# Kernel optimization log

Hardware: AMD Instinct MI355X
Metric: run time of the kernel (lower is better)

## Reference

```python
import jax, jax.numpy as jnp
import numpy as np

ATT_SCALE = 1.0

def setup_inputs() -> dict:
    key = jax.random.key(0)
    ks = jax.random.split(key, 9)
    N, Cin, Cout, E = 50000, 512, 512, 400000
    x = jax.random.normal(ks[0], (N, Cin), dtype=jnp.float32)
    eb = jax.random.randint(ks[1], (2, E), 0, N, dtype=jnp.int32)
    ev = jax.random.randint(ks[2], (2, E), 0, N, dtype=jnp.int32)
    ec = jax.random.randint(ks[3], (2, E), 0, N, dtype=jnp.int32)
    s = 1.0 / np.sqrt(Cin)
    W_bond = jax.random.normal(ks[4], (Cout, Cin), dtype=jnp.float32) * s
    W_vin = jax.random.normal(ks[5], (Cout, Cin), dtype=jnp.float32) * s
    W_vconn = jax.random.normal(ks[6], (Cout, Cin), dtype=jnp.float32) * s
    att_proj = jax.random.normal(ks[7], (Cout,), dtype=jnp.float32)
    bias = jnp.zeros((Cout,), dtype=jnp.float32)
    return {"x": x, "edge_index_bond": eb, "edge_index_virtual_intra": ev,
            "edge_index_virtual_conn": ec, "W_bond": W_bond, "W_vin": W_vin,
            "W_vconn": W_vconn, "att_proj": att_proj, "bias": bias}

def reference(x, edge_index_bond, edge_index_virtual_intra, edge_index_virtual_conn,
              W_bond, W_vin, W_vconn, att_proj, bias):
    N = x.shape[0]
    x_bond = x @ W_bond.T    # [N, Cout]
    x_vin = x @ W_vin.T
    x_vconn = x @ W_vconn.T

    # --- bond edges: add self loops, symmetric degree normalization ---
    loops = jnp.arange(N, dtype=edge_index_bond.dtype)
    row = jnp.concatenate([edge_index_bond[0], loops])
    col = jnp.concatenate([edge_index_bond[1], loops])
    deg = jax.ops.segment_sum(jnp.ones_like(row, dtype=x_bond.dtype), row, num_segments=N)
    dinv = jnp.where(deg > 0, deg ** -0.5, 0.0)
    norm = dinv[row] * dinv[col]                       # [E+N]
    out = jax.ops.segment_sum(x_bond[col] * norm[:, None], row, num_segments=N)

    # --- virtual intra edges: mean aggregation ---
    row_v, col_v = edge_index_virtual_intra[0], edge_index_virtual_intra[1]
    sum_vin = jax.ops.segment_sum(x_vin[col_v], row_v, num_segments=N)
    deg_vin = jnp.clip(jax.ops.segment_sum(jnp.ones_like(row_v, dtype=x_vin.dtype), row_v, num_segments=N), 1.0)
    out = out + sum_vin / deg_vin[:, None]

    # --- virtual conn edges: sigmoid dot-product attention ---
    row_c, col_c = edge_index_virtual_conn[0], edge_index_virtual_conn[1]
    proj_i = x_vconn[row_c] * att_proj
    proj_j = x_vconn[col_c] * att_proj
    alpha = jax.nn.sigmoid(jnp.sum(proj_i * proj_j, axis=-1) * ATT_SCALE)  # [E]
    out = out + jax.ops.segment_sum(alpha[:, None] * x_vconn[col_c], row_c, num_segments=N)

    return out + bias
```

## Files before the change

kernel.cpp:

```cpp
#include <hip/hip_runtime.h>
#include <hip/hip_fp8.h>
#include <stdint.h>

typedef _Float16 f16x8 __attribute__((ext_vector_type(8)));
typedef _Float16 f16x2 __attribute__((ext_vector_type(2)));
typedef float f32x4 __attribute__((ext_vector_type(4)));
typedef float f32x2 __attribute__((ext_vector_type(2)));

__device__ __forceinline__ unsigned short f2h(float f) {
    _Float16 h = (_Float16)f;
    return __builtin_bit_cast(unsigned short, h);
}
__device__ __forceinline__ float h2f(unsigned short s) {
    _Float16 h = __builtin_bit_cast(_Float16, s);
    return (float)h;
}

__device__ __forceinline__ unsigned pack_q4(float f0, float f1, float f2, float f3) {
#if __has_builtin(__builtin_amdgcn_cvt_pk_fp8_f32)
    unsigned u = (unsigned)__builtin_amdgcn_cvt_pk_fp8_f32(f0, f1, 0, false);
    u = (unsigned)__builtin_amdgcn_cvt_pk_fp8_f32(f2, f3, u, true);
    return u;
#else
    __hip_fp8_e4m3 q0(f0), q1(f1), q2(f2), q3(f3);
    return (unsigned)q0.__x | ((unsigned)q1.__x << 8) |
           ((unsigned)q2.__x << 16) | ((unsigned)q3.__x << 24);
#endif
}
__device__ __forceinline__ void add_q8(float* a, uint2 v, float s) {
#if __has_builtin(__builtin_amdgcn_cvt_pk_f32_fp8)
    f32x2 p0 = __builtin_amdgcn_cvt_pk_f32_fp8(v.x, false);
    f32x2 p1 = __builtin_amdgcn_cvt_pk_f32_fp8(v.x, true);
    f32x2 p2 = __builtin_amdgcn_cvt_pk_f32_fp8(v.y, false);
    f32x2 p3 = __builtin_amdgcn_cvt_pk_f32_fp8(v.y, true);
    a[0] += s * p0[0]; a[1] += s * p0[1];
    a[2] += s * p1[0]; a[3] += s * p1[1];
    a[4] += s * p2[0]; a[5] += s * p2[1];
    a[6] += s * p3[0]; a[7] += s * p3[1];
#else
    unsigned char b[8];
    *(uint2*)b = v;
    #pragma unroll
    for (int j = 0; j < 8; j++) {
        __hip_fp8_e4m3 q; q.__x = b[j];
        a[j] += s * (float)q;
    }
#endif
}

__device__ __forceinline__ void gload16(const void* g, void* lds) {
    __builtin_amdgcn_global_load_lds(
        (const __attribute__((address_space(1))) void*)g,
        (__attribute__((address_space(3))) void*)lds, 16, 0, 0);
}

#if __has_builtin(__builtin_amdgcn_fdot2)
__device__ __forceinline__ float dot2(f16x2 a, f16x2 b, float c) {
    return __builtin_amdgcn_fdot2(a, b, c, false);
}
#else
__device__ __forceinline__ float dot2(f16x2 a, f16x2 b, float c) {
    return c + (float)a[0] * (float)b[0] + (float)a[1] * (float)b[1];
}
#endif

__global__ __launch_bounds__(256) void k_prep(
    const float* __restrict__ x, unsigned short* __restrict__ xf,
    size_t valid, size_t total,
    const float* __restrict__ Wb, const float* __restrict__ Wv,
    const float* __restrict__ Wc, unsigned short* __restrict__ Wf,
    const int* __restrict__ eb, const int* __restrict__ ev, const int* __restrict__ ec,
    int Eb, int Ev, int Ec, int* __restrict__ cnt, int N)
{
    size_t i = (size_t)blockIdx.x * 256 + threadIdx.x;
    size_t idx = i * 4;
    if (idx < total) {
        ushort4 h;
        if (idx < valid) {
            float4 f = *(const float4*)(x + idx);
            h.x = f2h(f.x); h.y = f2h(f.y); h.z = f2h(f.z); h.w = f2h(f.w);
        } else {
            h.x = h.y = h.z = h.w = 0;
        }
        *(ushort4*)(xf + idx) = h;
    }
    if (idx < (size_t)1536 * 512) {
        int m = (int)(idx >> 9), k = (int)(idx & 511);
        const float* src;
        if (m < 512)       src = Wb + (size_t)m * 512 + k;
        else if (m < 1024) src = Wv + (size_t)(m - 512) * 512 + k;
        else               src = Wc + (size_t)(m - 1024) * 512 + k;
        float4 f = *(const float4*)src;
        ushort4 h;
        h.x = f2h(f.x); h.y = f2h(f.y); h.z = f2h(f.z); h.w = f2h(f.w);
        *(ushort4*)(Wf + idx) = h;
    }
    if (i < (size_t)(Eb + Ev + Ec)) {
        int ii = (int)i;
        if (ii < Eb) atomicAdd(cnt + eb[ii], 1);
        else if (ii < Eb + Ev) atomicAdd(cnt + N + ev[ii - Eb], 1);
        else atomicAdd(cnt + 2 * N + ec[ii - Eb - Ev], 1);
    }
}

__global__ __launch_bounds__(256) void k_scan_a(
    const int* __restrict__ cnt, int* __restrict__ ptr, int* __restrict__ bsum, int M)
{
    __shared__ int sh[256];
    int t = threadIdx.x;
    int base = blockIdx.x * 1024 + t * 4;
    int v[4];
    #pragma unroll
    for (int j = 0; j < 4; j++) v[j] = (base + j < M) ? cnt[base + j] : 0;
    int local = v[0] + v[1] + v[2] + v[3];
    sh[t] = local; __syncthreads();
    #pragma unroll
    for (int off = 1; off < 256; off <<= 1) {
        int x = (t >= off) ? sh[t - off] : 0;
        __syncthreads();
        sh[t] += x;
        __syncthreads();
    }
    int run = sh[t] - local;
    #pragma unroll
    for (int j = 0; j < 4; j++) {
        if (base + j < M) ptr[base + j] = run;
        run += v[j];
    }
    if (t == 255) bsum[blockIdx.x] = sh[255];
}

__global__ __launch_bounds__(256) void k_scan_b(int* __restrict__ bsum, int nb)
{
    __shared__ int sh[256];
    int t = threadIdx.x;
    int v = (t < nb) ? bsum[t] : 0;
    sh[t] = v; __syncthreads();
    #pragma unroll
    for (int off = 1; off < 256; off <<= 1) {
        int x = (t >= off) ? sh[t - off] : 0;
        __syncthreads();
        sh[t] += x;
        __syncthreads();
    }
    if (t < nb) bsum[t] = sh[t] - v;
}

__global__ __launch_bounds__(256) void k_scan_c(
    int* __restrict__ ptr, const int* __restrict__ bsum, int* __restrict__ cur,
    const int* __restrict__ cnt, float* __restrict__ dinv,
    int M, int N, int total)
{
    int idx = blockIdx.x * 256 + threadIdx.x;
    if (idx < M) {
        int p = ptr[idx] + bsum[idx >> 10];
        ptr[idx] = p;
        cur[idx] = p;
        if (idx < N) dinv[idx] = rsqrtf((float)(cnt[idx] + 1));
    }
    if (idx == 0) ptr[M] = total;
}

__global__ __launch_bounds__(256) void k_scatter3(
    const int* __restrict__ eb, const int* __restrict__ ev, const int* __restrict__ ec,
    int Eb, int Ev, int Ec, int* __restrict__ cur, int* __restrict__ cidx, int N)
{
    int i = blockIdx.x * 256 + threadIdx.x;
    const int* e; int il, off, E;
    if (i < Eb) { e = eb; il = i; off = 0; E = Eb; }
    else if (i < Eb + Ev) { e = ev; il = i - Eb; off = N; E = Ev; }
    else if (i < Eb + Ev + Ec) { e = ec; il = i - Eb - Ev; off = 2 * N; E = Ec; }
    else return;
    int r = e[il], c = e[E + il];
    int pos = atomicAdd(cur + off + r, 1);
    cidx[pos] = c;
}

__global__ __launch_bounds__(256) void k_gemm_f(
    const unsigned short* __restrict__ xf, const unsigned short* __restrict__ Wf,
    const float* __restrict__ dinv, int N,
    unsigned char* __restrict__ Ybv, unsigned short* __restrict__ Ycf)
{
    __shared__ uint4 As[2][1024];
    __shared__ uint4 Bs[2][1024];

    const int id = blockIdx.x;
    const int xcd = id & 7;
    const int jj = id >> 3;
    const int bn = jj % 12;
    const int bm = xcd + 8 * (jj / 12);

    const int t = threadIdx.x;
    const int lane = t & 63;
    const int w = t >> 6;
    const int wr = w >> 1;
    const int wc = w & 1;
    const int rA = lane >> 3;
    const int cs = lane & 7;

    f32x4 acc[4][4];
    #pragma unroll
    for (int i = 0; i < 4; i++)
        #pragma unroll
        for (int j = 0; j < 4; j++) acc[i][j] = (f32x4){0.f, 0.f, 0.f, 0.f};

    const size_t baseA = (size_t)bm * 128 * 512;
    const size_t baseB = (size_t)bn * 128 * 512;
    const int cg = cs ^ rA;

    #pragma unroll
    for (int j = 0; j < 4; j++) {
        int seg = w * 4 + j;
        int r = seg * 8 + rA;
        gload16(xf + baseA + (size_t)r * 512 + cg * 8, &As[0][seg * 64]);
        gload16(Wf + baseB + (size_t)r * 512 + cg * 8, &Bs[0][seg * 64]);
    }

    int cur = 0;
    for (int step = 0; step < 8; ++step) {
        if (step < 7) {
            int kt = (step + 1) * 64;
            #pragma unroll
            for (int j = 0; j < 4; j++) {
                int seg = w * 4 + j;
                int r = seg * 8 + rA;
                gload16(xf + baseA + (size_t)r * 512 + kt + cg * 8, &As[cur ^ 1][seg * 64]);
                gload16(Wf + baseB + (size_t)r * 512 + kt + cg * 8, &Bs[cur ^ 1][seg * 64]);
            }
            asm volatile("s_waitcnt vmcnt(8)" ::: "memory");
        } else {
            asm volatile("s_waitcnt vmcnt(0)" ::: "memory");
        }
        __builtin_amdgcn_sched_barrier(0);
        __builtin_amdgcn_s_barrier();

        #pragma unroll
        for (int kk = 0; kk < 2; kk++) {
            f16x8 a[4], b[4];
            #pragma unroll
            for (int ni = 0; ni < 4; ni++) {
                int ar = wr * 64 + ni * 16 + (lane & 15);
                int k8 = kk * 4 + (lane >> 4);
                a[ni] = __builtin_bit_cast(f16x8, As[cur][ar * 8 + (k8 ^ (ar & 7))]);
            }
            #pragma unroll
            for (int mi = 0; mi < 4; mi++) {
                int br = wc * 64 + mi * 16 + (lane & 15);
                int k8 = kk * 4 + (lane >> 4);
                b[mi] = __builtin_bit_cast(f16x8, Bs[cur][br * 8 + (k8 ^ (br & 7))]);
            }
            #pragma unroll
            for (int mi = 0; mi < 4; mi++)
                #pragma unroll
                for (int ni = 0; ni < 4; ni++)
                    acc[mi][ni] = __builtin_amdgcn_mfma_f32_16x16x32_f16(
                        b[mi], a[ni], acc[mi][ni], 0, 0, 0);
        }
        asm volatile("s_waitcnt lgkmcnt(0)" ::: "memory");
        __builtin_amdgcn_sched_barrier(0);
        __builtin_amdgcn_s_barrier();
        cur ^= 1;
    }

    const int nbase = bm * 128 + wr * 64 + (lane & 15);
    const int mq = wc * 64 + (lane >> 4) * 4;
    if (bn < 4) {
        #pragma unroll
        for (int ni = 0; ni < 4; ni++) {
            int n = nbase + ni * 16;
            float dv = (n < N) ? dinv[n] : 0.f;
            #pragma unroll
            for (int mi = 0; mi < 4; mi++) {
                int m0 = bn * 128 + mq + mi * 16;
                unsigned u = pack_q4(acc[mi][ni][0] * dv, acc[mi][ni][1] * dv,
                                     acc[mi][ni][2] * dv, acc[mi][ni][3] * dv);
                *(unsigned*)(Ybv + (size_t)n * 1024 + m0) = u;
            }
        }
    } else if (bn < 8) {
        #pragma unroll
        for (int ni = 0; ni < 4; ni++) {
            int n = nbase + ni * 16;
            #pragma unroll
            for (int mi = 0; mi < 4; mi++) {
                int m0 = bn * 128 + mq + mi * 16;
                unsigned u = pack_q4(acc[mi][ni][0], acc[mi][ni][1],
                                     acc[mi][ni][2], acc[mi][ni][3]);
                *(unsigned*)(Ybv + (size_t)n * 1024 + m0) = u;
            }
        }
    } else {
        #pragma unroll
        for (int ni = 0; ni < 4; ni++) {
            int n = nbase + ni * 16;
            #pragma unroll
            for (int mi = 0; mi < 4; mi++) {
                int m0 = (bn - 8) * 128 + mq + mi * 16;
                ushort4 h;
                h.x = f2h(acc[mi][ni][0]); h.y = f2h(acc[mi][ni][1]);
                h.z = f2h(acc[mi][ni][2]); h.w = f2h(acc[mi][ni][3]);
                *(ushort4*)(Ycf + (size_t)n * 512 + m0) = h;
            }
        }
    }
}

__device__ __forceinline__ void acc_h8(float* a, uint4 v, float s) {
    a[0] += s * h2f((unsigned short)(v.x & 0xffff));
    a[1] += s * h2f((unsigned short)(v.x >> 16));
    a[2] += s * h2f((unsigned short)(v.y & 0xffff));
    a[3] += s * h2f((unsigned short)(v.y >> 16));
    a[4] += s * h2f((unsigned short)(v.z & 0xffff));
    a[5] += s * h2f((unsigned short)(v.z >> 16));
    a[6] += s * h2f((unsigned short)(v.w & 0xffff));
    a[7] += s * h2f((unsigned short)(v.w >> 16));
}
__device__ __forceinline__ float dot8(const f16x2* ph, uint4 u) {
    float d = 0.f;
    d = dot2(ph[0], __builtin_bit_cast(f16x2, u.x), d);
    d = dot2(ph[1], __builtin_bit_cast(f16x2, u.y), d);
    d = dot2(ph[2], __builtin_bit_cast(f16x2, u.z), d);
    d = dot2(ph[3], __builtin_bit_cast(f16x2, u.w), d);
    return d;
}

__global__ __launch_bounds__(256) void k_gather(
    const int* __restrict__ ptr, const int* __restrict__ cidx,
    const float* __restrict__ dinv,
    const unsigned char* __restrict__ Ybv, const unsigned short* __restrict__ Ycf,
    const float* __restrict__ att, const float* __restrict__ bias,
    float* __restrict__ out, int N)
{
    int node = blockIdx.x * 4 + (threadIdx.x >> 6);
    if (node >= N) return;
    int lane = threadIdx.x & 63;

    float di = dinv[node];
    float a[8] = {0.f, 0.f, 0.f, 0.f, 0.f, 0.f, 0.f, 0.f};

    {
        uint2 v = *((const uint2*)(Ybv + (size_t)node * 1024) + lane);
        add_q8(a, v, 1.0f);
    }
    {
        int e0 = ptr[node], e1 = ptr[node + 1];
        int e = e0;
        for (; e + 4 <= e1; e += 4) {
            int c0 = cidx[e], c1 = cidx[e + 1], c2 = cidx[e + 2], c3 = cidx[e + 3];
            uint2 v0 = *((const uint2*)(Ybv + (size_t)c0 * 1024) + lane);
            uint2 v1 = *((const uint2*)(Ybv + (size_t)c1 * 1024) + lane);
            uint2 v2 = *((const uint2*)(Ybv + (size_t)c2 * 1024) + lane);
            uint2 v3 = *((const uint2*)(Ybv + (size_t)c3 * 1024) + lane);
            add_q8(a, v0, 1.0f); add_q8(a, v1, 1.0f);
            add_q8(a, v2, 1.0f); add_q8(a, v3, 1.0f);
        }
        for (; e < e1; ++e) {
            int c = cidx[e];
            uint2 v = *((const uint2*)(Ybv + (size_t)c * 1024) + lane);
            add_q8(a, v, 1.0f);
        }
    }
    {
        const float4* bp = (const float4*)(bias + lane * 8);
        float4 q0 = bp[0], q1 = bp[1];
        a[0] = a[0] * di + q0.x; a[1] = a[1] * di + q0.y;
        a[2] = a[2] * di + q0.z; a[3] = a[3] * di + q0.w;
        a[4] = a[4] * di + q1.x; a[5] = a[5] * di + q1.y;
        a[6] = a[6] * di + q1.z; a[7] = a[7] * di + q1.w;
    }
    {
        int e0 = ptr[N + node], e1 = ptr[N + node + 1];
        float vsc = 1.0f / (float)((e1 - e0) > 1 ? (e1 - e0) : 1);
        int e = e0;
        for (; e + 4 <= e1; e += 4) {
            int c0 = cidx[e], c1 = cidx[e + 1], c2 = cidx[e + 2], c3 = cidx[e + 3];
            uint2 v0 = *((const uint2*)(Ybv + (size_t)c0 * 1024 + 512) + lane);
            uint2 v1 = *((const uint2*)(Ybv + (size_t)c1 * 1024 + 512) + lane);
            uint2 v2 = *((const uint2*)(Ybv + (size_t)c2 * 1024 + 512) + lane);
            uint2 v3 = *((const uint2*)(Ybv + (size_t)c3 * 1024 + 512) + lane);
            add_q8(a, v0, vsc); add_q8(a, v1, vsc);
            add_q8(a, v2, vsc); add_q8(a, v3, vsc);
        }
        for (; e < e1; ++e) {
            int c = cidx[e];
            uint2 v = *((const uint2*)(Ybv + (size_t)c * 1024 + 512) + lane);
            add_q8(a, v, vsc);
        }
    }
    {
        int e0 = ptr[2 * N + node], e1 = ptr[2 * N + node + 1];
        if (e0 < e1) {
            const float4* ap = (const float4*)att + lane * 2;
            float4 t0 = ap[0], t1 = ap[1];
            float yr[8];
            {
                uint4 u = *((const uint4*)(Ycf + (size_t)node * 512) + lane);
                yr[0] = h2f((unsigned short)(u.x & 0xffff));
                yr[1] = h2f((unsigned short)(u.x >> 16));
                yr[2] = h2f((unsigned short)(u.y & 0xffff));
                yr[3] = h2f((unsigned short)(u.y >> 16));
                yr[4] = h2f((unsigned short)(u.z & 0xffff));
                yr[5] = h2f((unsigned short)(u.z >> 16));
                yr[6] = h2f((unsigned short)(u.w & 0xffff));
                yr[7] = h2f((unsigned short)(u.w >> 16));
            }
            f16x2 ph[4];
            ph[0] = (f16x2){(_Float16)(yr[0] * t0.x * t0.x), (_Float16)(yr[1] * t0.y * t0.y)};
            ph[1] = (f16x2){(_Float16)(yr[2] * t0.z * t0.z), (_Float16)(yr[3] * t0.w * t0.w)};
            ph[2] = (f16x2){(_Float16)(yr[4] * t1.x * t1.x), (_Float16)(yr[5] * t1.y * t1.y)};
            ph[3] = (f16x2){(_Float16)(yr[6] * t1.z * t1.z), (_Float16)(yr[7] * t1.w * t1.w)};
            int e = e0;
            for (; e + 4 <= e1; e += 4) {
                int c0 = cidx[e], c1 = cidx[e + 1], c2 = cidx[e + 2], c3 = cidx[e + 3];
                uint4 u0 = *((const uint4*)(Ycf + (size_t)c0 * 512) + lane);
                uint4 u1 = *((const uint4*)(Ycf + (size_t)c1 * 512) + lane);
                uint4 u2 = *((const uint4*)(Ycf + (size_t)c2 * 512) + lane);
                uint4 u3 = *((const uint4*)(Ycf + (size_t)c3 * 512) + lane);
                float d0 = dot8(ph, u0);
                float d1 = dot8(ph, u1);
                float d2 = dot8(ph, u2);
                float d3 = dot8(ph, u3);
                #pragma unroll
                for (int off = 32; off > 0; off >>= 1) {
                    d0 += __shfl_xor(d0, off);
                    d1 += __shfl_xor(d1, off);
                    d2 += __shfl_xor(d2, off);
                    d3 += __shfl_xor(d3, off);
                }
                float al0 = 1.0f / (1.0f + __expf(-d0));
                float al1 = 1.0f / (1.0f + __expf(-d1));
                float al2 = 1.0f / (1.0f + __expf(-d2));
                float al3 = 1.0f / (1.0f + __expf(-d3));
                acc_h8(a, u0, al0); acc_h8(a, u1, al1);
                acc_h8(a, u2, al2); acc_h8(a, u3, al3);
            }
            for (; e < e1; ++e) {
                int c = cidx[e];
                uint4 u = *((const uint4*)(Ycf + (size_t)c * 512) + lane);
                float dot = dot8(ph, u);
                #pragma unroll
                for (int off = 32; off > 0; off >>= 1) dot += __shfl_xor(dot, off);
                float alpha = 1.0f / (1.0f + __expf(-dot));
                acc_h8(a, u, alpha);
            }
        }
    }
    f32x4 o0 = (f32x4){a[0], a[1], a[2], a[3]};
    f32x4 o1 = (f32x4){a[4], a[5], a[6], a[7]};
    f32x4* dst = (f32x4*)(out + (size_t)node * 512 + lane * 8);
    __builtin_nontemporal_store(o0, dst);
    __builtin_nontemporal_store(o1, dst + 1);
}

extern "C" void kernel_launch(void* const* d_in, const int* in_sizes, int n_in,
                              void* d_out, int out_size, void* d_ws, size_t ws_size,
                              hipStream_t stream) {
    const float* x    = (const float*)d_in[0];
    const int*   eb   = (const int*)d_in[1];
    const int*   ev   = (const int*)d_in[2];
    const int*   ec   = (const int*)d_in[3];
    const float* Wb   = (const float*)d_in[4];
    const float* Wv   = (const float*)d_in[5];
    const float* Wc   = (const float*)d_in[6];
    const float* att  = (const float*)d_in[7];
    const float* bias = (const float*)d_in[8];
    float* out = (float*)d_out;

    const int N  = in_sizes[0] / 512;
    const int Eb = in_sizes[1] / 2;
    const int Ev = in_sizes[2] / 2;
    const int Ec = in_sizes[3] / 2;
    const int Etot = Eb + Ev + Ec;
    const int nbm = (((N + 127) / 128 + 7) / 8) * 8;
    const size_t Npad = (size_t)nbm * 128;
    const int M = 3 * N;
    const int nScanBlocks = (M + 1023) / 1024;

    char* p = (char*)d_ws;
    unsigned char*  Ybv = (unsigned char*)p;  p += Npad * 1024;
    unsigned short* Ycf = (unsigned short*)p; p += Npad * 512 * 2;
    unsigned short* Wf  = (unsigned short*)p; p += (size_t)1536 * 512 * 2;
    unsigned short* xf  = (unsigned short*)p; p += Npad * 512 * 2;
    int* cnt  = (int*)p; p += ((size_t)M * 4 + 255) & ~(size_t)255;
    int* ptr_ = (int*)p; p += ((size_t)(M + 1) * 4 + 255) & ~(size_t)255;
    int* cur  = (int*)p; p += ((size_t)M * 4 + 255) & ~(size_t)255;
    int* bsum = (int*)p; p += 256 * 4;
    int* cidx = (int*)p; p += ((size_t)Etot * 4 + 255) & ~(size_t)255;
    float* dinv = (float*)p; p += ((size_t)N * 4 + 255) & ~(size_t)255;

    const size_t total = Npad * 512, valid = (size_t)N * 512;

    hipMemsetAsync(cnt, 0, (size_t)M * 4, stream);
    k_prep<<<(int)((total / 4 + 255) / 256), 256, 0, stream>>>(
        x, xf, valid, total, Wb, Wv, Wc, Wf, eb, ev, ec, Eb, Ev, Ec, cnt, N);

    k_scan_a<<<nScanBlocks, 256, 0, stream>>>(cnt, ptr_, bsum, M);
    k_scan_b<<<1, 256, 0, stream>>>(bsum, nScanBlocks);
    k_scan_c<<<(M + 255) / 256, 256, 0, stream>>>(ptr_, bsum, cur, cnt, dinv, M, N, Etot);
    k_scatter3<<<(Etot + 255) / 256, 256, 0, stream>>>(eb, ev, ec, Eb, Ev, Ec, cur, cidx, N);

    k_gemm_f<<<nbm * 12, 256, 0, stream>>>(xf, Wf, dinv, N, Ybv, Ycf);

    k_gather<<<(N + 3) / 4, 256, 0, stream>>>(ptr_, cidx, dinv, Ybv, Ycf, att, bias, out, N);
}
```

Measured before the change: 394.6 us.

## Load GEMM B operand directly to registers, fuse block scan, deepen gather unroll

The GEMM now loads the weight tile straight from global memory into double-buffered registers instead of staging it through LDS. This removes the B shared-memory writes and reads and halves LDS use, at the cost of more VGPRs and uncoalesced per-lane 16-byte loads. The separate block-sum scan kernel is folded into k_scan_c, where every block redundantly rescans the block sums, saving one launch. The gather loops for bond and intra edges are unrolled to 8 outstanding loads to raise memory-level parallelism.

New measurement: 476.4 us. 20.7% more time.

```diff
diff --git a/kernel.cpp b/kernel.cpp
--- a/kernel.cpp
+++ b/kernel.cpp
@@ -130,30 +130,26 @@
     if (t == 255) bsum[blockIdx.x] = sh[255];
 }
 
-__global__ __launch_bounds__(256) void k_scan_b(int* __restrict__ bsum, int nb)
-{
-    __shared__ int sh[256];
-    int t = threadIdx.x;
-    int v = (t < nb) ? bsum[t] : 0;
-    sh[t] = v; __syncthreads();
-    #pragma unroll
-    for (int off = 1; off < 256; off <<= 1) {
-        int x = (t >= off) ? sh[t - off] : 0;
-        __syncthreads();
-        sh[t] += x;
-        __syncthreads();
-    }
-    if (t < nb) bsum[t] = sh[t] - v;
-}
-
 __global__ __launch_bounds__(256) void k_scan_c(
     int* __restrict__ ptr, const int* __restrict__ bsum, int* __restrict__ cur,
     const int* __restrict__ cnt, float* __restrict__ dinv,
-    int M, int N, int total)
+    int M, int N, int total, int nb)
 {
-    int idx = blockIdx.x * 256 + threadIdx.x;
+    __shared__ int raw[256], scn[256];
+    int t = threadIdx.x;
+    int v = (t < nb) ? bsum[t] : 0;
+    raw[t] = v; scn[t] = v; __syncthreads();
+    #pragma unroll
+    for (int off = 1; off < 256; off <<= 1) {
+        int x = (t >= off) ? scn[t - off] : 0;
+        __syncthreads();
+        scn[t] += x;
+        __syncthreads();
+    }
+    int idx = blockIdx.x * 256 + t;
     if (idx < M) {
-        int p = ptr[idx] + bsum[idx >> 10];
+        int blk = idx >> 10;
+        int p = ptr[idx] + (scn[blk] - raw[blk]);
         ptr[idx] = p;
         cur[idx] = p;
         if (idx < N) dinv[idx] = rsqrtf((float)(cnt[idx] + 1));
@@ -182,7 +178,6 @@
     unsigned char* __restrict__ Ybv, unsigned short* __restrict__ Ycf)
 {
     __shared__ uint4 As[2][1024];
-    __shared__ uint4 Bs[2][1024];
 
     const int id = blockIdx.x;
     const int xcd = id & 7;
@@ -205,29 +200,43 @@
         for (int j = 0; j < 4; j++) acc[i][j] = (f32x4){0.f, 0.f, 0.f, 0.f};
 
     const size_t baseA = (size_t)bm * 128 * 512;
-    const size_t baseB = (size_t)bn * 128 * 512;
     const int cg = cs ^ rA;
+
+    const unsigned short* bbase =
+        Wf + ((size_t)bn * 128 + wc * 64 + (lane & 15)) * 512 + (lane >> 4) * 8;
 
     #pragma unroll
     for (int j = 0; j < 4; j++) {
         int seg = w * 4 + j;
         int r = seg * 8 + rA;
         gload16(xf + baseA + (size_t)r * 512 + cg * 8, &As[0][seg * 64]);
-        gload16(Wf + baseB + (size_t)r * 512 + cg * 8, &Bs[0][seg * 64]);
-    }
-
-    int cur = 0;
-    for (int step = 0; step < 8; ++step) {
-        if (step < 7) {
-            int kt = (step + 1) * 64;
+    }
+    f16x8 b0[2][4], b1[2][4];
+    #pragma unroll
+    for (int kk = 0; kk < 2; kk++)
+        #pragma unroll
+        for (int mi = 0; mi < 4; mi++)
+            b0[kk][mi] = *(const f16x8*)(bbase + (size_t)mi * 8192 + kk * 32);
+
+    #pragma unroll
+    for (int s = 0; s < 8; ++s) {
+        const int cur = s & 1;
+        f16x8 (&bc)[2][4] = (s & 1) ? b1 : b0;
+        f16x8 (&bnx)[2][4] = (s & 1) ? b0 : b1;
+        if (s < 7) {
+            const int kt = (s + 1) * 64;
             #pragma unroll
             for (int j = 0; j < 4; j++) {
                 int seg = w * 4 + j;
                 int r = seg * 8 + rA;
                 gload16(xf + baseA + (size_t)r * 512 + kt + cg * 8, &As[cur ^ 1][seg * 64]);
-                gload16(Wf + baseB + (size_t)r * 512 + kt + cg * 8, &Bs[cur ^ 1][seg * 64]);
-            }
-            asm volatile("s_waitcnt vmcnt(8)" ::: "memory");
+            }
+            #pragma unroll
+            for (int kk = 0; kk < 2; kk++)
+                #pragma unroll
+                for (int mi = 0; mi < 4; mi++)
+                    bnx[kk][mi] = *(const f16x8*)(bbase + (size_t)mi * 8192 + kt + kk * 32);
+            asm volatile("s_waitcnt vmcnt(12)" ::: "memory");
         } else {
             asm volatile("s_waitcnt vmcnt(0)" ::: "memory");
         }
@@ -236,7 +245,7 @@
 
         #pragma unroll
         for (int kk = 0; kk < 2; kk++) {
-            f16x8 a[4], b[4];
+            f16x8 a[4];
             #pragma unroll
             for (int ni = 0; ni < 4; ni++) {
                 int ar = wr * 64 + ni * 16 + (lane & 15);
@@ -244,22 +253,15 @@
                 a[ni] = __builtin_bit_cast(f16x8, As[cur][ar * 8 + (k8 ^ (ar & 7))]);
             }
             #pragma unroll
-            for (int mi = 0; mi < 4; mi++) {
-                int br = wc * 64 + mi * 16 + (lane & 15);
-                int k8 = kk * 4 + (lane >> 4);
-                b[mi] = __builtin_bit_cast(f16x8, Bs[cur][br * 8 + (k8 ^ (br & 7))]);
-            }
-            #pragma unroll
             for (int mi = 0; mi < 4; mi++)
                 #pragma unroll
                 for (int ni = 0; ni < 4; ni++)
                     acc[mi][ni] = __builtin_amdgcn_mfma_f32_16x16x32_f16(
-                        b[mi], a[ni], acc[mi][ni], 0, 0, 0);
+                        bc[kk][mi], a[ni], acc[mi][ni], 0, 0, 0);
         }
         asm volatile("s_waitcnt lgkmcnt(0)" ::: "memory");
         __builtin_amdgcn_sched_barrier(0);
         __builtin_amdgcn_s_barrier();
-        cur ^= 1;
     }
 
     const int nbase = bm * 128 + wr * 64 + (lane & 15);
@@ -345,18 +347,16 @@
     {
         int e0 = ptr[node], e1 = ptr[node + 1];
         int e = e0;
-        for (; e + 4 <= e1; e += 4) {
-            int c0 = cidx[e], c1 = cidx[e + 1], c2 = cidx[e + 2], c3 = cidx[e + 3];
-            uint2 v0 = *((const uint2*)(Ybv + (size_t)c0 * 1024) + lane);
-            uint2 v1 = *((const uint2*)(Ybv + (size_t)c1 * 1024) + lane);
-            uint2 v2 = *((const uint2*)(Ybv + (size_t)c2 * 1024) + lane);
-            uint2 v3 = *((const uint2*)(Ybv + (size_t)c3 * 1024) + lane);
-            add_q8(a, v0, 1.0f); add_q8(a, v1, 1.0f);
-            add_q8(a, v2, 1.0f); add_q8(a, v3, 1.0f);
+        for (; e + 8 <= e1; e += 8) {
+            uint2 v[8];
+            #pragma unroll
+            for (int j = 0; j < 8; j++)
+                v[j] = *((const uint2*)(Ybv + (size_t)cidx[e + j] * 1024) + lane);
+            #pragma unroll
+            for (int j = 0; j < 8; j++) add_q8(a, v[j], 1.0f);
         }
         for (; e < e1; ++e) {
-            int c = cidx[e];
-            uint2 v = *((const uint2*)(Ybv + (size_t)c * 1024) + lane);
+            uint2 v = *((const uint2*)(Ybv + (size_t)cidx[e] * 1024) + lane);
             add_q8(a, v, 1.0f);
         }
     }
@@ -372,18 +372,16 @@
         int e0 = ptr[N + node], e1 = ptr[N + node + 1];
         float vsc = 1.0f / (float)((e1 - e0) > 1 ? (e1 - e0) : 1);
         int e = e0;
-        for (; e + 4 <= e1; e += 4) {
-            int c0 = cidx[e], c1 = cidx[e + 1], c2 = cidx[e + 2], c3 = cidx[e + 3];
-            uint2 v0 = *((const uint2*)(Ybv + (size_t)c0 * 1024 + 512) + lane);
-            uint2 v1 = *((const uint2*)(Ybv + (size_t)c1 * 1024 + 512) + lane);
-            uint2 v2 = *((const uint2*)(Ybv + (size_t)c2 * 1024 + 512) + lane);
-            uint2 v3 = *((const uint2*)(Ybv + (size_t)c3 * 1024 + 512) + lane);
-            add_q8(a, v0, vsc); add_q8(a, v1, vsc);
-            add_q8(a, v2, vsc); add_q8(a, v3, vsc);
+        for (; e + 8 <= e1; e += 8) {
+            uint2 v[8];
+            #pragma unroll
+            for (int j = 0; j < 8; j++)
+                v[j] = *((const uint2*)(Ybv + (size_t)cidx[e + j] * 1024 + 512) + lane);
+            #pragma unroll
+            for (int j = 0; j < 8; j++) add_q8(a, v[j], vsc);
         }
         for (; e < e1; ++e) {
-            int c = cidx[e];
-            uint2 v = *((const uint2*)(Ybv + (size_t)c * 1024 + 512) + lane);
+            uint2 v = *((const uint2*)(Ybv + (size_t)cidx[e] * 1024 + 512) + lane);
             add_q8(a, v, vsc);
         }
     }
@@ -495,8 +493,7 @@
         x, xf, valid, total, Wb, Wv, Wc, Wf, eb, ev, ec, Eb, Ev, Ec, cnt, N);
 
     k_scan_a<<<nScanBlocks, 256, 0, stream>>>(cnt, ptr_, bsum, M);
-    k_scan_b<<<1, 256, 0, stream>>>(bsum, nScanBlocks);
-    k_scan_c<<<(M + 255) / 256, 256, 0, stream>>>(ptr_, bsum, cur, cnt, dinv, M, N, Etot);
+    k_scan_c<<<(M + 255) / 256, 256, 0, stream>>>(ptr_, bsum, cur, cnt, dinv, M, N, Etot, nScanBlocks);
     k_scatter3<<<(Etot + 255) / 256, 256, 0, stream>>>(eb, ev, ec, Eb, Ev, Ec, cur, cidx, N);
 
     k_gemm_f<<<nbm * 12, 256, 0, stream>>>(xf, Wf, dinv, N, Ybv, Ycf);
```
